# Performance work log

Measured on AMD Instinct MI355X. Metric: run time of the kernel, lower is better.

Reference implementation:

```python
import jax, jax.numpy as jnp
import numpy as np

N_NODES = 100000
IN_C = 300
OUT_C = 200
N_EDGES = 1600000
NEG_SLOPE = 0.2  # PyG GATConv default


def setup_inputs() -> dict:
    key = jax.random.key(0)
    ks = jax.random.split(key, 12)
    x = jax.random.normal(ks[0], (N_NODES, IN_C), dtype=jnp.float32)
    edge_index = jax.random.randint(ks[1], (2, N_EDGES), 0, N_NODES, dtype=jnp.int64)
    s0 = 1.0 / np.sqrt(IN_C)
    s1 = 1.0 / np.sqrt(OUT_C)
    return {
        "x": x,
        "W0": jax.random.normal(ks[2], (IN_C, OUT_C), dtype=jnp.float32) * s0,
        "a_src0": jax.random.normal(ks[3], (OUT_C,), dtype=jnp.float32) * s1,
        "a_dst0": jax.random.normal(ks[4], (OUT_C,), dtype=jnp.float32) * s1,
        "b0": jnp.zeros((OUT_C,), dtype=jnp.float32),
        "W1": jax.random.normal(ks[5], (OUT_C, OUT_C), dtype=jnp.float32) * s1,
        "a_src1": jax.random.normal(ks[6], (OUT_C,), dtype=jnp.float32) * s1,
        "a_dst1": jax.random.normal(ks[7], (OUT_C,), dtype=jnp.float32) * s1,
        "b1": jnp.zeros((OUT_C,), dtype=jnp.float32),
        "edge_index": edge_index,
    }


def _gat_conv(x, W, a_src, a_dst, b, src, dst, n):
    # h: [N, F'] projected features
    h = x @ W
    alpha_src = h @ a_src  # [N]
    alpha_dst = h @ a_dst  # [N]
    # per-edge raw attention score, message flows src -> dst
    e = jax.nn.leaky_relu(alpha_src[src] + alpha_dst[dst], NEG_SLOPE)  # [E]
    # segment softmax over incoming edges of each destination node
    m = jax.ops.segment_max(e, dst, num_segments=n)
    ex = jnp.exp(e - m[dst])
    denom = jax.ops.segment_sum(ex, dst, num_segments=n)
    alpha = ex / denom[dst]  # [E]
    # scatter-add weighted messages
    out = jax.ops.segment_sum(h[src] * alpha[:, None], dst, num_segments=n)
    return out + b


def reference(x, W0, a_src0, a_dst0, b0, W1, a_src1, a_dst1, b1, edge_index):
    n = x.shape[0]
    # PyG GATConv default: add self-loops
    loops = jnp.arange(n, dtype=edge_index.dtype)
    src = jnp.concatenate([edge_index[0], loops])
    dst = jnp.concatenate([edge_index[1], loops])
    h = jax.nn.relu(_gat_conv(x, W0, a_src0, a_dst0, b0, src, dst, n))
    h = jax.nn.relu(_gat_conv(h, W1, a_src1, a_dst1, b1, src, dst, n))
    return h
```

## Files before the change

### kernel.cpp

```cpp
#include <hip/hip_runtime.h>

#define IN_C 300
#define OUT_C 200
#define NEG_SLOPE 0.2f

#define BMB 64
#define BMW 16
#define BKC 20

static inline int cdiv(long a, int b) { return (int)((a + b - 1) / b); }

__device__ __forceinline__ void glds16(const float* g, float* l) {
  __builtin_amdgcn_global_load_lds(
      (const __attribute__((address_space(1))) void*)g,
      (__attribute__((address_space(3))) void*)l, 16, 0, 0);
}

__global__ __launch_bounds__(256)
void zero_int_kernel(int* __restrict__ p, int n) {
  int i = blockIdx.x * blockDim.x + threadIdx.x;
  if (i < n) p[i] = 0;
}

__device__ __forceinline__ void edge_sd(const int* __restrict__ src,
                                        const int* __restrict__ dst,
                                        int i, int E, int& s, int& d) {
  if (i < E) { s = src[i]; d = dst[i]; } else { s = d = i - E; }
}

__global__ __launch_bounds__(256)
void padw_kernel(const float* __restrict__ W, float* __restrict__ Wpad, int K) {
  int idx = blockIdx.x * blockDim.x + threadIdx.x;
  if (idx >= K * 64) return;
  int k = idx >> 6, c = (idx & 63) * 4;
  float4 v = make_float4(0.f, 0.f, 0.f, 0.f);
  if (c < OUT_C) v = *(const float4*)(W + (long)k * OUT_C + c);
  *(float4*)(Wpad + (long)k * 256 + c) = v;
}

__global__ __launch_bounds__(256)
void hist_kernel(const int* __restrict__ src, const int* __restrict__ dst,
                 int E, int ET, int* __restrict__ counts) {
  int i = blockIdx.x * blockDim.x + threadIdx.x;
  if (i >= ET) return;
  int s, d; edge_sd(src, dst, i, E, s, d);
  atomicAdd(counts + d, 1);
}

__global__ __launch_bounds__(256)
void scan_a_kernel(const int* __restrict__ in, int n, int* __restrict__ out,
                   int* __restrict__ bsums) {
  __shared__ int lds[256];
  int t = threadIdx.x;
  int base = blockIdx.x * 1024 + t * 4;
  int v0 = (base + 0 < n) ? in[base + 0] : 0;
  int v1 = (base + 1 < n) ? in[base + 1] : 0;
  int v2 = (base + 2 < n) ? in[base + 2] : 0;
  int v3 = (base + 3 < n) ? in[base + 3] : 0;
  int s1 = v0 + v1, s2 = s1 + v2, s3 = s2 + v3;
  lds[t] = s3;
  __syncthreads();
  for (int o = 1; o < 256; o <<= 1) {
    int x = (t >= o) ? lds[t - o] : 0;
    __syncthreads();
    lds[t] += x;
    __syncthreads();
  }
  int pre = (t > 0) ? lds[t - 1] : 0;
  if (base + 0 < n) out[base + 0] = pre + v0;
  if (base + 1 < n) out[base + 1] = pre + s1;
  if (base + 2 < n) out[base + 2] = pre + s2;
  if (base + 3 < n) out[base + 3] = pre + s3;
  if (t == 255) bsums[blockIdx.x] = lds[255];
}

__global__ __launch_bounds__(256)
void scan_b_kernel(int* __restrict__ bs, int nb) {
  __shared__ int lds[256];
  int t = threadIdx.x;
  lds[t] = (t < nb) ? bs[t] : 0;
  __syncthreads();
  for (int o = 1; o < 256; o <<= 1) {
    int x = (t >= o) ? lds[t - o] : 0;
    __syncthreads();
    lds[t] += x;
    __syncthreads();
  }
  if (t < nb) bs[t] = lds[t];
}

__global__ __launch_bounds__(256)
void scan_c_kernel(int* __restrict__ out, int n, const int* __restrict__ bs) {
  int i = blockIdx.x * blockDim.x + threadIdx.x;
  if (i >= n) return;
  int b = i >> 10;
  if (b > 0) out[i] += bs[b - 1];
}

__global__ __launch_bounds__(256)
void fill_kernel(const int* __restrict__ src, const int* __restrict__ dst,
                 int E, int ET, const int* __restrict__ rowptr,
                 int* __restrict__ cursor, int* __restrict__ csr_src) {
  int i = blockIdx.x * blockDim.x + threadIdx.x;
  if (i >= ET) return;
  int s, d; edge_sd(src, dst, i, E, s, d);
  int pos = rowptr[d] + atomicAdd(cursor + d, 1);
  csr_src[pos] = s;
}

__global__ __launch_bounds__(256)
void gemm_ws_kernel(const float* __restrict__ A, const float* __restrict__ Wpad,
                    const float* __restrict__ a_src, const float* __restrict__ a_dst,
                    float* __restrict__ H, float* __restrict__ asN,
                    float* __restrict__ adN, int K, int N) {
  __shared__ float Ws[BKC][256];
  __shared__ float As[BMB][BKC];
  int t = threadIdx.x;
  int wave = t >> 6, lane = t & 63;
  int col = lane * 4;
  long row0 = (long)blockIdx.x * BMB;
  int wrow = wave * BMW;

  float4 acc[BMW];
  #pragma unroll
  for (int r = 0; r < BMW; ++r) acc[r] = make_float4(0.f, 0.f, 0.f, 0.f);

  const int nch = K / BKC;
  for (int ch = 0; ch < nch; ++ch) {
    const int kc = ch * BKC;
    #pragma unroll
    for (int j = 0; j < 5; ++j) {
      int r = wave * 5 + j;
      glds16(Wpad + (long)(kc + r) * 256 + col, &Ws[r][0]);
    }
    {
      int f = wave * 64 + lane;
      long row = row0 + f / 5;
      if (row >= N) row = N - 1;
      glds16(A + row * K + kc + (f % 5) * 4, &As[0][0] + wave * 256);
    }
    if (wave == 0) {
      int f = 256 + lane;
      long row = row0 + f / 5;
      if (row >= N) row = N - 1;
      glds16(A + row * K + kc + (f % 5) * 4, &As[0][0] + 1024);
    }
    __syncthreads();
    #pragma unroll
    for (int kk = 0; kk < BKC; kk += 4) {
      float4 w0 = *(float4*)&Ws[kk + 0][col];
      float4 w1 = *(float4*)&Ws[kk + 1][col];
      float4 w2 = *(float4*)&Ws[kk + 2][col];
      float4 w3 = *(float4*)&Ws[kk + 3][col];
      #pragma unroll
      for (int r = 0; r < BMW; ++r) {
        float4 a = *(float4*)&As[wrow + r][kk];
        acc[r].x += a.x * w0.x + a.y * w1.x + a.z * w2.x + a.w * w3.x;
        acc[r].y += a.x * w0.y + a.y * w1.y + a.z * w2.y + a.w * w3.y;
        acc[r].z += a.x * w0.z + a.y * w1.z + a.z * w2.z + a.w * w3.z;
        acc[r].w += a.x * w0.w + a.y * w1.w + a.z * w2.w + a.w * w3.w;
      }
    }
    __syncthreads();
  }

  bool cok = col < OUT_C;
  #pragma unroll
  for (int r = 0; r < BMW; ++r) {
    long grow = row0 + wrow + r;
    if (cok && grow < N) *(float4*)(H + grow * OUT_C + col) = acc[r];
  }
  float4 vs = make_float4(0.f, 0.f, 0.f, 0.f);
  float4 vd = make_float4(0.f, 0.f, 0.f, 0.f);
  if (cok) {
    vs = *(const float4*)(a_src + col);
    vd = *(const float4*)(a_dst + col);
  }
  #pragma unroll
  for (int r = 0; r < BMW; ++r) {
    float ss = acc[r].x * vs.x + acc[r].y * vs.y + acc[r].z * vs.z + acc[r].w * vs.w;
    float sd = acc[r].x * vd.x + acc[r].y * vd.y + acc[r].z * vd.z + acc[r].w * vd.w;
    #pragma unroll
    for (int o = 32; o > 0; o >>= 1) {
      ss += __shfl_xor(ss, o);
      sd += __shfl_xor(sd, o);
    }
    long grow = row0 + wrow + r;
    if (lane == 0 && grow < N) { asN[grow] = ss; adN[grow] = sd; }
  }
}

__global__ __launch_bounds__(256)
void gather_agg_kernel(const float* __restrict__ h, const float* __restrict__ asN,
                       const float* __restrict__ adN, const int* __restrict__ rowptr,
                       const int* __restrict__ csr_src, const float* __restrict__ bias,
                       float* __restrict__ out, int N) {
  int wid = (int)(((long)blockIdx.x * blockDim.x + threadIdx.x) >> 6);
  int lane = threadIdx.x & 63;
  if (wid >= N) return;
  int start = rowptr[wid], end = rowptr[wid + 1];
  float ad = adN[wid];

  float m = -1e30f;
  for (int j = start + lane; j < end; j += 64) {
    float sc = asN[csr_src[j]] + ad;
    sc = sc > 0.f ? sc : NEG_SLOPE * sc;
    m = fmaxf(m, sc);
  }
  for (int o = 32; o > 0; o >>= 1) m = fmaxf(m, __shfl_xor(m, o));
  float se = 0.f;
  for (int j = start + lane; j < end; j += 64) {
    float sc = asN[csr_src[j]] + ad;
    sc = sc > 0.f ? sc : NEG_SLOPE * sc;
    se += __expf(sc - m);
  }
  for (int o = 32; o > 0; o >>= 1) se += __shfl_xor(se, o);
  float inv = 1.0f / se;

  float acc0 = 0.f, acc1 = 0.f, acc2 = 0.f, acc3 = 0.f;
  int c0 = lane, c1 = lane + 64, c2 = lane + 128, c3 = lane + 192;
  for (int j = start; j < end; ++j) {
    int s = csr_src[j];
    float sc = asN[s] + ad;
    sc = sc > 0.f ? sc : NEG_SLOPE * sc;
    float w = __expf(sc - m) * inv;
    const float* hrow = h + (long)s * OUT_C;
    acc0 += w * hrow[c0];
    acc1 += w * hrow[c1];
    acc2 += w * hrow[c2];
    if (c3 < OUT_C) acc3 += w * hrow[c3];
  }
  float* orow = out + (long)wid * OUT_C;
  orow[c0] = fmaxf(acc0 + bias[c0], 0.f);
  orow[c1] = fmaxf(acc1 + bias[c1], 0.f);
  orow[c2] = fmaxf(acc2 + bias[c2], 0.f);
  if (c3 < OUT_C) orow[c3] = fmaxf(acc3 + bias[c3], 0.f);
}

static void run_layer(const float* xin, int K, const float* Wpad,
                      const float* a_s, const float* a_d, const float* b,
                      const int* rowptr, const int* csr_src, int N,
                      float* hbuf, float* asN, float* adN, float* outbuf,
                      hipStream_t stream) {
  gemm_ws_kernel<<<cdiv(N, BMB), 256, 0, stream>>>(xin, Wpad, a_s, a_d,
                                                   hbuf, asN, adN, K, N);
  gather_agg_kernel<<<cdiv((long)N * 64, 256), 256, 0, stream>>>(
      hbuf, asN, adN, rowptr, csr_src, b, outbuf, N);
}

extern "C" void kernel_launch(void* const* d_in, const int* in_sizes, int n_in,
                              void* d_out, int out_size, void* d_ws, size_t ws_size,
                              hipStream_t stream) {
  const float* x   = (const float*)d_in[0];
  const float* W0  = (const float*)d_in[1];
  const float* as0 = (const float*)d_in[2];
  const float* ad0 = (const float*)d_in[3];
  const float* b0  = (const float*)d_in[4];
  const float* W1  = (const float*)d_in[5];
  const float* as1 = (const float*)d_in[6];
  const float* ad1 = (const float*)d_in[7];
  const float* b1  = (const float*)d_in[8];
  const int*   ei  = (const int*)d_in[9];

  const int N  = in_sizes[0] / IN_C;
  const int E  = in_sizes[9] / 2;
  const int ET = E + N;
  const int* src = ei;
  const int* dst = ei + E;

  float* out = (float*)d_out;

  char* ws = (char*)d_ws;
  float* hbuf   = (float*)ws;
  float* asN    = (float*)(ws + (size_t)N * OUT_C * 4);
  float* adN    = asN + N;
  int*   rowptr = (int*)(adN + N);
  int*   counts = rowptr + (N + 1);
  int*   bsums  = counts + N;
  int*   csrsrc = bsums + 256;
  size_t woff = ((size_t)(csrsrc + ET - (int*)ws) + 3) & ~(size_t)3;
  float* wpad0 = (float*)ws + woff;
  float* wpad1 = wpad0 + (size_t)IN_C * 256;

  const int nb = cdiv(N, 1024);

  padw_kernel<<<cdiv(IN_C * 64, 256), 256, 0, stream>>>(W0, wpad0, IN_C);
  padw_kernel<<<cdiv(OUT_C * 64, 256), 256, 0, stream>>>(W1, wpad1, OUT_C);
  zero_int_kernel<<<cdiv(N, 256), 256, 0, stream>>>(counts, N);
  hist_kernel<<<cdiv(ET, 256), 256, 0, stream>>>(src, dst, E, ET, counts);
  scan_a_kernel<<<nb, 256, 0, stream>>>(counts, N, rowptr + 1, bsums);
  scan_b_kernel<<<1, 256, 0, stream>>>(bsums, nb);
  scan_c_kernel<<<cdiv(N, 256), 256, 0, stream>>>(rowptr + 1, N, bsums);
  zero_int_kernel<<<1, 256, 0, stream>>>(rowptr, 1);
  zero_int_kernel<<<cdiv(N, 256), 256, 0, stream>>>(counts, N);
  fill_kernel<<<cdiv(ET, 256), 256, 0, stream>>>(src, dst, E, ET, rowptr, counts, csrsrc);

  run_layer(x, IN_C, wpad0, as0, ad0, b0, rowptr, csrsrc, N, hbuf, asN, adN, out, stream);
  run_layer(out, OUT_C, wpad1, as1, ad1, b1, rowptr, csrsrc, N, hbuf, asN, adN, out, stream);
}
```

Baseline: 1.321 ms.

## Double-buffer GEMM LDS staging and unroll gather aggregation by two edges

The projection GEMM now uses two LDS buffers, issuing the async global-to-LDS loads for the next K chunk before computing the current one. This lets loads overlap with math and drops one barrier per chunk. The gather-aggregate loop processes two neighbor edges per iteration to expose more memory-level parallelism. It also moves the softmax normalization out of the loop into a single multiply at the end. The cost is double the shared memory in the GEMM, which may reduce occupancy, and a correctness dependency on the global_load_lds completion ordering relative to the single barrier.

```diff
diff --git a/kernel.cpp b/kernel.cpp
--- a/kernel.cpp
+++ b/kernel.cpp
@@ -113,55 +113,69 @@
                     const float* __restrict__ a_src, const float* __restrict__ a_dst,
                     float* __restrict__ H, float* __restrict__ asN,
                     float* __restrict__ adN, int K, int N) {
-  __shared__ float Ws[BKC][256];
-  __shared__ float As[BMB][BKC];
+  __shared__ float Ws[2][BKC][256];
+  __shared__ float As[2][BMB][BKC];
   int t = threadIdx.x;
   int wave = t >> 6, lane = t & 63;
   int col = lane * 4;
   long row0 = (long)blockIdx.x * BMB;
   int wrow = wave * BMW;
 
+  const float* sW = Wpad + (long)(wave * 5) * 256 + col;
+  int f0 = wave * 64 + lane;
+  long ar0 = row0 + f0 / 5; if (ar0 >= N) ar0 = N - 1;
+  const float* sA0 = A + ar0 * K + (f0 % 5) * 4;
+  int f1 = 256 + lane;
+  long ar1 = row0 + f1 / 5; if (ar1 >= N) ar1 = N - 1;
+  const float* sA1 = A + ar1 * K + (f1 % 5) * 4;
+
+  auto stage = [&](int buf) {
+    #pragma unroll
+    for (int j = 0; j < 5; ++j)
+      glds16(sW + j * 256, &Ws[buf][wave * 5 + j][0]);
+    glds16(sA0, &As[buf][0][0] + wave * 256);
+    if (wave == 0) glds16(sA1, &As[buf][0][0] + 1024);
+    sW += BKC * 256; sA0 += BKC; sA1 += BKC;
+  };
+
   float4 acc[BMW];
   #pragma unroll
   for (int r = 0; r < BMW; ++r) acc[r] = make_float4(0.f, 0.f, 0.f, 0.f);
 
   const int nch = K / BKC;
+  stage(0);
+  int cur = 0;
   for (int ch = 0; ch < nch; ++ch) {
-    const int kc = ch * BKC;
-    #pragma unroll
-    for (int j = 0; j < 5; ++j) {
-      int r = wave * 5 + j;
-      glds16(Wpad + (long)(kc + r) * 256 + col, &Ws[r][0]);
-    }
-    {
-      int f = wave * 64 + lane;
-      long row = row0 + f / 5;
-      if (row >= N) row = N - 1;
-      glds16(A + row * K + kc + (f % 5) * 4, &As[0][0] + wave * 256);
-    }
-    if (wave == 0) {
-      int f = 256 + lane;
-      long row = row0 + f / 5;
-      if (row >= N) row = N - 1;
-      glds16(A + row * K + kc + (f % 5) * 4, &As[0][0] + 1024);
-    }
-    __syncthreads();
+    __syncthreads();
+    if (ch + 1 < nch) stage(cur ^ 1);
     #pragma unroll
     for (int kk = 0; kk < BKC; kk += 4) {
-      float4 w0 = *(float4*)&Ws[kk + 0][col];
-      float4 w1 = *(float4*)&Ws[kk + 1][col];
-      float4 w2 = *(float4*)&Ws[kk + 2][col];
-      float4 w3 = *(float4*)&Ws[kk + 3][col];
+      float4 w0 = *(float4*)&Ws[cur][kk + 0][col];
+      float4 w1 = *(float4*)&Ws[cur][kk + 1][col];
+      float4 w2 = *(float4*)&Ws[cur][kk + 2][col];
+      float4 w3 = *(float4*)&Ws[cur][kk + 3][col];
       #pragma unroll
       for (int r = 0; r < BMW; ++r) {
-        float4 a = *(float4*)&As[wrow + r][kk];
-        acc[r].x += a.x * w0.x + a.y * w1.x + a.z * w2.x + a.w * w3.x;
-        acc[r].y += a.x * w0.y + a.y * w1.y + a.z * w2.y + a.w * w3.y;
-        acc[r].z += a.x * w0.z + a.y * w1.z + a.z * w2.z + a.w * w3.z;
-        acc[r].w += a.x * w0.w + a.y * w1.w + a.z * w2.w + a.w * w3.w;
+        float4 a = *(float4*)&As[cur][wrow + r][kk];
+        acc[r].x = fmaf(a.x, w0.x, acc[r].x);
+        acc[r].x = fmaf(a.y, w1.x, acc[r].x);
+        acc[r].x = fmaf(a.z, w2.x, acc[r].x);
+        acc[r].x = fmaf(a.w, w3.x, acc[r].x);
+        acc[r].y = fmaf(a.x, w0.y, acc[r].y);
+        acc[r].y = fmaf(a.y, w1.y, acc[r].y);
+        acc[r].y = fmaf(a.z, w2.y, acc[r].y);
+        acc[r].y = fmaf(a.w, w3.y, acc[r].y);
+        acc[r].z = fmaf(a.x, w0.z, acc[r].z);
+        acc[r].z = fmaf(a.y, w1.z, acc[r].z);
+        acc[r].z = fmaf(a.z, w2.z, acc[r].z);
+        acc[r].z = fmaf(a.w, w3.z, acc[r].z);
+        acc[r].w = fmaf(a.x, w0.w, acc[r].w);
+        acc[r].w = fmaf(a.y, w1.w, acc[r].w);
+        acc[r].w = fmaf(a.z, w2.w, acc[r].w);
+        acc[r].w = fmaf(a.w, w3.w, acc[r].w);
       }
     }
-    __syncthreads();
+    cur ^= 1;
   }
 
   bool cok = col < OUT_C;
@@ -219,22 +233,36 @@
 
   float acc0 = 0.f, acc1 = 0.f, acc2 = 0.f, acc3 = 0.f;
   int c0 = lane, c1 = lane + 64, c2 = lane + 128, c3 = lane + 192;
-  for (int j = start; j < end; ++j) {
-    int s = csr_src[j];
-    float sc = asN[s] + ad;
-    sc = sc > 0.f ? sc : NEG_SLOPE * sc;
-    float w = __expf(sc - m) * inv;
-    const float* hrow = h + (long)s * OUT_C;
-    acc0 += w * hrow[c0];
-    acc1 += w * hrow[c1];
-    acc2 += w * hrow[c2];
-    if (c3 < OUT_C) acc3 += w * hrow[c3];
+  int j = start;
+  for (; j + 2 <= end; j += 2) {
+    int s0 = csr_src[j], s1 = csr_src[j + 1];
+    float e0 = asN[s0] + ad, e1 = asN[s1] + ad;
+    e0 = e0 > 0.f ? e0 : NEG_SLOPE * e0;
+    e1 = e1 > 0.f ? e1 : NEG_SLOPE * e1;
+    float w0 = __expf(e0 - m), w1 = __expf(e1 - m);
+    const float* h0 = h + (long)s0 * OUT_C;
+    const float* h1 = h + (long)s1 * OUT_C;
+    acc0 = fmaf(w0, h0[c0], acc0); acc0 = fmaf(w1, h1[c0], acc0);
+    acc1 = fmaf(w0, h0[c1], acc1); acc1 = fmaf(w1, h1[c1], acc1);
+    acc2 = fmaf(w0, h0[c2], acc2); acc2 = fmaf(w1, h1[c2], acc2);
+    if (c3 < OUT_C) { acc3 = fmaf(w0, h0[c3], acc3); acc3 = fmaf(w1, h1[c3], acc3); }
+  }
+  if (j < end) {
+    int s0 = csr_src[j];
+    float e0 = asN[s0] + ad;
+    e0 = e0 > 0.f ? e0 : NEG_SLOPE * e0;
+    float w0 = __expf(e0 - m);
+    const float* h0 = h + (long)s0 * OUT_C;
+    acc0 = fmaf(w0, h0[c0], acc0);
+    acc1 = fmaf(w0, h0[c1], acc1);
+    acc2 = fmaf(w0, h0[c2], acc2);
+    if (c3 < OUT_C) acc3 = fmaf(w0, h0[c3], acc3);
   }
   float* orow = out + (long)wid * OUT_C;
-  orow[c0] = fmaxf(acc0 + bias[c0], 0.f);
-  orow[c1] = fmaxf(acc1 + bias[c1], 0.f);
-  orow[c2] = fmaxf(acc2 + bias[c2], 0.f);
-  if (c3 < OUT_C) orow[c3] = fmaxf(acc3 + bias[c3], 0.f);
+  orow[c0] = fmaxf(fmaf(acc0, inv, bias[c0]), 0.f);
+  orow[c1] = fmaxf(fmaf(acc1, inv, bias[c1]), 0.f);
+  orow[c2] = fmaxf(fmaf(acc2, inv, bias[c2]), 0.f);
+  if (c3 < OUT_C) orow[c3] = fmaxf(fmaf(acc3, inv, bias[c3]), 0.f);
 }
 
 static void run_layer(const float* xin, int K, const float* Wpad,
```

Result: faster. 1.134 ms (-14.2%).
